# Performance work log

Measured on AMD Instinct MI355X. Metric: run time of the kernel, lower is better.

The kernel has to match this reference:

```python
import jax, jax.numpy as jnp
import numpy as np

B, T, D = 32, 1024, 1024
PCA_DIM = 256
NS = 4
NC = 1024
SEC = PCA_DIM // NS


def setup_inputs() -> dict:
    key = jax.random.key(0)
    k1, k2, k3 = jax.random.split(key, 3)
    inputs = jax.random.normal(k1, (B, T, D), dtype=jnp.float32)
    # variance_scaling(1.0, 'fan_avg', 'normal'): std = sqrt(2 / (fan_in + fan_out))
    pca_proj = jax.random.normal(k2, (D, PCA_DIM), dtype=jnp.float32) * np.float32(np.sqrt(2.0 / (D + PCA_DIM)))
    pre_bias = jnp.zeros((1, D), dtype=jnp.float32)
    # per-section codebooks, variance_scaling(0.1, 'fan_avg', 'normal')
    codebooks = jax.random.normal(k3, (NS, NC, SEC), dtype=jnp.float32) * np.float32(np.sqrt(0.1 * 2.0 / (NC + SEC)))
    return {"inputs": inputs, "pca_proj": pca_proj, "pre_bias": pre_bias, "codebooks": codebooks}


def reference(inputs, pca_proj, pre_bias, codebooks):
    in_shape = inputs.shape
    d = in_shape[-1]
    flat = inputs.reshape(-1, d)  # [N, D]
    n = flat.shape[0]
    # --- PCA projection + reconstruction / decorrelation losses ---
    projected = (flat + pre_bias) @ pca_proj            # [N, P]
    unprojected = projected @ pca_proj.T - pre_bias     # [N, D]
    l2_loss = jnp.mean(jnp.sqrt(jnp.sum(jnp.square(flat - unprojected), axis=-1)))
    cov = projected.T @ projected / n                   # [P, P]
    cov_loss = jnp.mean(jnp.square(cov - jnp.eye(pca_proj.shape[1], dtype=projected.dtype)))
    pca_loss = l2_loss + cov_loss
    # --- per-section vector quantization ---
    ns, nc, sec = codebooks.shape
    secs = projected.reshape(n, ns, sec).transpose(1, 0, 2)  # [ns, N, sec] == jnp.split along -1

    def quantize_section(x, cb):
        # x: [N, sec], cb: [nc, sec]; squared-L2 cdist via expansion
        dist = (jnp.sum(x * x, axis=1, keepdims=True)
                - 2.0 * (x @ cb.T)
                + jnp.sum(cb * cb, axis=1)[None, :])    # [N, nc]
        idx = jnp.argmin(dist, axis=1)                  # [N]
        q = cb[idx]                                     # gather == one_hot @ cb
        loss = jnp.square(q - jax.lax.stop_gradient(x))  # [N, sec]
        q_st = x + jax.lax.stop_gradient(q - x)         # straight-through
        return q_st, loss, idx

    q, sec_loss, idx = jax.vmap(quantize_section)(secs, codebooks)  # [ns,N,sec] x2, [ns,N]
    quantized = q.transpose(1, 0, 2).reshape(n, ns * sec)           # concat sections -> [N, P]
    quantized = (quantized @ pca_proj.T - pre_bias).reshape(in_shape)  # pca_unproject
    nn_idx = idx.reshape((ns,) + in_shape[:-1])                     # [ns, B, T]
    quantization_loss = jnp.mean(sec_loss.reshape((ns,) + in_shape[:-1] + (sec,)), axis=0) + pca_loss
    codebook = jax.lax.stop_gradient(codebooks.reshape(ns * nc, sec))
    cluster_counts = jnp.ones((ns, nc), dtype=jnp.float32)  # eval mode: jnp.ones init, no EMA
    return quantized, quantization_loss, nn_idx, codebook, cluster_counts
```

## Files before the change

### kernel.cpp

```cpp
#include <hip/hip_runtime.h>
#include <math.h>

#define NROW 32768
#define DIM  1024
#define PDIM 256
#define NSEC 4
#define NCODE 1024
#define SECD 64

__global__ __launch_bounds__(256) void k_proj(const float* __restrict__ X,
                                              const float* __restrict__ W,
                                              const float* __restrict__ bias,
                                              float* __restrict__ proj) {
    __shared__ float As[16][64];
    __shared__ float Bs[16][64];
    const int t = threadIdx.x;
    const int tx = t & 15, ty = t >> 4;
    const int rb = blockIdx.y * 64;
    const int cbase = blockIdx.x * 64;
    const int lr = t >> 2;
    const int lk = (t & 3) * 4;
    const int bk = t >> 4;
    const int bc = (t & 15) * 4;
    float acc[4][4] = {};
    float part[4][4] = {};
    for (int kc = 0; kc < DIM; kc += 16) {
        if (kc == 384) {
            #pragma unroll
            for (int i = 0; i < 4; ++i)
                #pragma unroll
                for (int j = 0; j < 4; ++j) { part[i][j] = acc[i][j]; acc[i][j] = 0.0f; }
        } else if (kc == 768) {
            #pragma unroll
            for (int i = 0; i < 4; ++i)
                #pragma unroll
                for (int j = 0; j < 4; ++j) { part[i][j] = __fadd_rn(part[i][j], acc[i][j]); acc[i][j] = 0.0f; }
        }
        float4 av = *(const float4*)&X[(size_t)(rb + lr) * DIM + kc + lk];
        float4 bb = *(const float4*)&bias[kc + lk];
        av.x += bb.x; av.y += bb.y; av.z += bb.z; av.w += bb.w;
        float4 bv = *(const float4*)&W[(size_t)(kc + bk) * PDIM + cbase + bc];
        As[lk + 0][lr] = av.x; As[lk + 1][lr] = av.y;
        As[lk + 2][lr] = av.z; As[lk + 3][lr] = av.w;
        *(float4*)&Bs[bk][bc] = bv;
        __syncthreads();
        #pragma unroll
        for (int k = 0; k < 16; ++k) {
            float4 a4 = *(const float4*)&As[k][ty * 4];
            float4 b4 = *(const float4*)&Bs[k][tx * 4];
            float aa[4] = {a4.x, a4.y, a4.z, a4.w};
            float bbv[4] = {b4.x, b4.y, b4.z, b4.w};
            #pragma unroll
            for (int i = 0; i < 4; ++i)
                #pragma unroll
                for (int j = 0; j < 4; ++j)
                    acc[i][j] = fmaf(aa[i], bbv[j], acc[i][j]);
        }
        __syncthreads();
    }
    #pragma unroll
    for (int i = 0; i < 4; ++i) {
        float r[4];
        #pragma unroll
        for (int j = 0; j < 4; ++j) r[j] = __fadd_rn(part[i][j], acc[i][j]);
        float4 v = make_float4(r[0], r[1], r[2], r[3]);
        *(float4*)&proj[(size_t)(rb + ty * 4 + i) * PDIM + cbase + tx * 4] = v;
    }
}

__global__ __launch_bounds__(256) void k_cov(const float* __restrict__ Pm,
                                             float* __restrict__ cov) {
    __shared__ float As[16][64];
    __shared__ float Bs[16][64];
    const int t = threadIdx.x;
    const int tx = t & 15, ty = t >> 4;
    const int ib = blockIdx.x * 64;
    const int jb = blockIdx.y * 64;
    const int nb = blockIdx.z * 2048;
    const int sk = t >> 4;
    const int sc = (t & 15) * 4;
    float acc[4][4] = {};
    for (int kc = 0; kc < 2048; kc += 16) {
        float4 a = *(const float4*)&Pm[(size_t)(nb + kc + sk) * PDIM + ib + sc];
        float4 b = *(const float4*)&Pm[(size_t)(nb + kc + sk) * PDIM + jb + sc];
        *(float4*)&As[sk][sc] = a;
        *(float4*)&Bs[sk][sc] = b;
        __syncthreads();
        #pragma unroll
        for (int k = 0; k < 16; ++k) {
            float4 a4 = *(const float4*)&As[k][ty * 4];
            float4 b4 = *(const float4*)&Bs[k][tx * 4];
            float aa[4] = {a4.x, a4.y, a4.z, a4.w};
            float bb[4] = {b4.x, b4.y, b4.z, b4.w};
            #pragma unroll
            for (int i = 0; i < 4; ++i)
                #pragma unroll
                for (int j = 0; j < 4; ++j)
                    acc[i][j] = fmaf(aa[i], bb[j], acc[i][j]);
        }
        __syncthreads();
    }
    #pragma unroll
    for (int i = 0; i < 4; ++i)
        #pragma unroll
        for (int j = 0; j < 4; ++j)
            atomicAdd(&cov[(size_t)(ib + ty * 4 + i) * PDIM + jb + tx * 4 + j], acc[i][j]);
}

__global__ __launch_bounds__(256) void k_covloss(const float* __restrict__ cov,
                                                 float* __restrict__ scal) {
    const int t = threadIdx.x;
    float s = 0.0f;
    for (int e = t; e < PDIM * PDIM; e += 256) {
        int i = e >> 8, j = e & 255;
        float v = cov[e] * (1.0f / 32768.0f) - (i == j ? 1.0f : 0.0f);
        s = fmaf(v, v, s);
    }
    #pragma unroll
    for (int o = 1; o < 64; o <<= 1) s += __shfl_xor(s, o);
    __shared__ float r4[4];
    if ((t & 63) == 0) r4[t >> 6] = s;
    __syncthreads();
    if (t == 0) scal[1] = (r4[0] + r4[1] + r4[2] + r4[3]) * (1.0f / 65536.0f);
}

__global__ __launch_bounds__(256) void k_unproj_res(const float* __restrict__ Pm,
                                                    const float* __restrict__ W,
                                                    const float* __restrict__ X,
                                                    const float* __restrict__ bias,
                                                    float* __restrict__ rowres) {
    __shared__ float As[16][64];
    __shared__ float Bs[16][64];
    const int t = threadIdx.x;
    const int tx = t & 15, ty = t >> 4;
    const int rb = blockIdx.y * 64;
    const int db = blockIdx.x * 64;
    const int lr = t >> 2;
    const int lk = (t & 3) * 4;
    float acc[4][4] = {};
    for (int kc = 0; kc < PDIM; kc += 16) {
        float4 a = *(const float4*)&Pm[(size_t)(rb + lr) * PDIM + kc + lk];
        float4 b = *(const float4*)&W[(size_t)(db + lr) * PDIM + kc + lk];
        As[lk + 0][lr] = a.x; As[lk + 1][lr] = a.y;
        As[lk + 2][lr] = a.z; As[lk + 3][lr] = a.w;
        Bs[lk + 0][lr] = b.x; Bs[lk + 1][lr] = b.y;
        Bs[lk + 2][lr] = b.z; Bs[lk + 3][lr] = b.w;
        __syncthreads();
        #pragma unroll
        for (int k = 0; k < 16; ++k) {
            float4 a4 = *(const float4*)&As[k][ty * 4];
            float4 b4 = *(const float4*)&Bs[k][tx * 4];
            float aa[4] = {a4.x, a4.y, a4.z, a4.w};
            float bb[4] = {b4.x, b4.y, b4.z, b4.w};
            #pragma unroll
            for (int i = 0; i < 4; ++i)
                #pragma unroll
                for (int j = 0; j < 4; ++j)
                    acc[i][j] = fmaf(aa[i], bb[j], acc[i][j]);
        }
        __syncthreads();
    }
    float4 b4 = *(const float4*)&bias[db + tx * 4];
    float bb[4] = {b4.x, b4.y, b4.z, b4.w};
    #pragma unroll
    for (int i = 0; i < 4; ++i) {
        const int row = rb + ty * 4 + i;
        float4 x4 = *(const float4*)&X[(size_t)row * DIM + db + tx * 4];
        float xx[4] = {x4.x, x4.y, x4.z, x4.w};
        float part = 0.0f;
        #pragma unroll
        for (int j = 0; j < 4; ++j) {
            float diff = xx[j] + bb[j] - acc[i][j];
            part = fmaf(diff, diff, part);
        }
        #pragma unroll
        for (int o = 1; o < 16; o <<= 1) part += __shfl_xor(part, o);
        if (tx == 0) atomicAdd(&rowres[row], part);
    }
}

__global__ __launch_bounds__(256) void k_l2(const float* __restrict__ rowres,
                                            float* __restrict__ scal) {
    int r = blockIdx.x * 256 + threadIdx.x;
    float v = sqrtf(rowres[r]);
    #pragma unroll
    for (int o = 1; o < 64; o <<= 1) v += __shfl_xor(v, o);
    if ((threadIdx.x & 63) == 0) atomicAdd(&scal[0], v);
}

__global__ __launch_bounds__(256) void k_cnorm(const float* __restrict__ cbs,
                                               float* __restrict__ cnorm) {
    int c = blockIdx.x * 256 + threadIdx.x;
    const float* p = &cbs[(size_t)c * SECD];
    float a[8];
    #pragma unroll
    for (int j = 0; j < 8; ++j) a[j] = __fmul_rn(p[j], p[j]);
    #pragma unroll
    for (int i = 8; i < 64; i += 8)
        #pragma unroll
        for (int j = 0; j < 8; ++j)
            a[j] = __fadd_rn(a[j], __fmul_rn(p[i + j], p[i + j]));
    float r = __fadd_rn(__fadd_rn(__fadd_rn(a[0], a[1]), __fadd_rn(a[2], a[3])),
                        __fadd_rn(__fadd_rn(a[4], a[5]), __fadd_rn(a[6], a[7])));
    cnorm[c] = r;
}

__global__ __launch_bounds__(256) void k_vq(const float* __restrict__ proj,
                                            const float* __restrict__ cbs,
                                            const float* __restrict__ cnorm,
                                            int* __restrict__ widx,
                                            float* __restrict__ out_idx,
                                            float* __restrict__ out_qloss) {
    __shared__ float xs[64][64];
    __shared__ float cs[64][64];
    __shared__ float xnorm[64];
    __shared__ int   sidx[64];
    __shared__ float qlds[64][65];
    const int t = threadIdx.x;
    const int tx = t & 15, ty = t >> 4;
    const int rb = blockIdx.x * 64;
    const int lr = t >> 2;
    const int kq = (t & 3) * 16;

    for (int e = t; e < 64 * 65; e += 256) (&qlds[0][0])[e] = 0.0f;

    for (int s = 0; s < NSEC; ++s) {
        #pragma unroll
        for (int i = 0; i < 16; i += 4) {
            float4 v = *(const float4*)&proj[(size_t)(rb + lr) * PDIM + s * SECD + kq + i];
            xs[kq + i + 0][lr] = v.x; xs[kq + i + 1][lr] = v.y;
            xs[kq + i + 2][lr] = v.z; xs[kq + i + 3][lr] = v.w;
        }
        __syncthreads();
        if (t < 64) {
            float a[8];
            #pragma unroll
            for (int j = 0; j < 8; ++j) { float v = xs[j][t]; a[j] = __fmul_rn(v, v); }
            #pragma unroll
            for (int i = 8; i < 64; i += 8)
                #pragma unroll
                for (int j = 0; j < 8; ++j) {
                    float v = xs[i + j][t];
                    a[j] = __fadd_rn(a[j], __fmul_rn(v, v));
                }
            xnorm[t] = __fadd_rn(__fadd_rn(__fadd_rn(a[0], a[1]), __fadd_rn(a[2], a[3])),
                                 __fadd_rn(__fadd_rn(a[4], a[5]), __fadd_rn(a[6], a[7])));
        }
        float best[4]; int bidx[4];
        #pragma unroll
        for (int i = 0; i < 4; ++i) { best[i] = 3.4e38f; bidx[i] = 0; }

        for (int ct = 0; ct < 16; ++ct) {
            __syncthreads();
            #pragma unroll
            for (int i = 0; i < 16; i += 4) {
                float4 v = *(const float4*)&cbs[(size_t)(s * NCODE + ct * 64 + lr) * SECD + kq + i];
                cs[kq + i + 0][lr] = v.x; cs[kq + i + 1][lr] = v.y;
                cs[kq + i + 2][lr] = v.z; cs[kq + i + 3][lr] = v.w;
            }
            __syncthreads();
            float4 cn4 = *(const float4*)&cnorm[s * NCODE + ct * 64 + tx * 4];
            float cna[4] = {cn4.x, cn4.y, cn4.z, cn4.w};
            float acc[4][4] = {};
            #pragma unroll 16
            for (int k = 0; k < 64; ++k) {
                float4 a4 = *(const float4*)&xs[k][ty * 4];
                float4 b4 = *(const float4*)&cs[k][tx * 4];
                float aa[4] = {a4.x, a4.y, a4.z, a4.w};
                float bb[4] = {b4.x, b4.y, b4.z, b4.w};
                #pragma unroll
                for (int i = 0; i < 4; ++i)
                    #pragma unroll
                    for (int j = 0; j < 4; ++j)
                        acc[i][j] = fmaf(aa[i], bb[j], acc[i][j]);
            }
            #pragma unroll
            for (int i = 0; i < 4; ++i) {
                float xn = xnorm[ty * 4 + i];
                #pragma unroll
                for (int j = 0; j < 4; ++j) {
                    float d = __fadd_rn(__fsub_rn(xn, __fmul_rn(2.0f, acc[i][j])), cna[j]);
                    int code = ct * 64 + tx * 4 + j;
                    if (d < best[i]) { best[i] = d; bidx[i] = code; }
                }
            }
        }
        #pragma unroll
        for (int i = 0; i < 4; ++i) {
            float d = best[i]; int ix = bidx[i];
            #pragma unroll
            for (int o = 1; o < 16; o <<= 1) {
                float od = __shfl_xor(d, o);
                int   oi = __shfl_xor(ix, o);
                if (od < d || (od == d && oi < ix)) { d = od; ix = oi; }
            }
            if (tx == 0) {
                int row = rb + ty * 4 + i;
                widx[s * NROW + row] = ix;
                out_idx[s * NROW + row] = (float)ix;
                sidx[ty * 4 + i] = ix;
            }
        }
        __syncthreads();
        {
            const float* crow = &cbs[(size_t)(s * NCODE + sidx[lr]) * SECD];
            #pragma unroll
            for (int i = 0; i < 16; i += 4) {
                float4 q = *(const float4*)&crow[kq + i];
                float qq[4] = {q.x, q.y, q.z, q.w};
                #pragma unroll
                for (int u = 0; u < 4; ++u) {
                    float d = qq[u] - xs[kq + i + u][lr];
                    qlds[lr][kq + i + u] += d * d;
                }
            }
        }
        __syncthreads();
    }
    for (int e = t; e < 4096; e += 256) {
        int r = e >> 6, j = e & 63;
        out_qloss[(size_t)(rb + r) * SECD + j] = 0.25f * qlds[r][j];
    }
}

__global__ __launch_bounds__(256) void k_cbu(const float* __restrict__ cbs,
                                             const float* __restrict__ W,
                                             float* __restrict__ cbu) {
    __shared__ float As[16][64];
    __shared__ float Bs[16][64];
    const int t = threadIdx.x;
    const int tx = t & 15, ty = t >> 4;
    const int s = blockIdx.z;
    const int cbase = blockIdx.y * 64;
    const int db = blockIdx.x * 64;
    const int lr = t >> 2;
    const int lk = (t & 3) * 4;
    float acc[4][4] = {};
    for (int kc = 0; kc < SECD; kc += 16) {
        float4 a = *(const float4*)&cbs[(size_t)(s * NCODE + cbase + lr) * SECD + kc + lk];
        float4 b = *(const float4*)&W[(size_t)(db + lr) * PDIM + s * SECD + kc + lk];
        As[lk + 0][lr] = a.x; As[lk + 1][lr] = a.y;
        As[lk + 2][lr] = a.z; As[lk + 3][lr] = a.w;
        Bs[lk + 0][lr] = b.x; Bs[lk + 1][lr] = b.y;
        Bs[lk + 2][lr] = b.z; Bs[lk + 3][lr] = b.w;
        __syncthreads();
        #pragma unroll
        for (int k = 0; k < 16; ++k) {
            float4 a4 = *(const float4*)&As[k][ty * 4];
            float4 b4 = *(const float4*)&Bs[k][tx * 4];
            float aa[4] = {a4.x, a4.y, a4.z, a4.w};
            float bb[4] = {b4.x, b4.y, b4.z, b4.w};
            #pragma unroll
            for (int i = 0; i < 4; ++i)
                #pragma unroll
                for (int j = 0; j < 4; ++j)
                    acc[i][j] = fmaf(aa[i], bb[j], acc[i][j]);
        }
        __syncthreads();
    }
    #pragma unroll
    for (int i = 0; i < 4; ++i) {
        float4 v = make_float4(acc[i][0], acc[i][1], acc[i][2], acc[i][3]);
        *(float4*)&cbu[(size_t)(s * NCODE + cbase + ty * 4 + i) * DIM + db + tx * 4] = v;
    }
}

__global__ __launch_bounds__(256) void k_gather(const float* __restrict__ cbu,
                                                const int* __restrict__ widx,
                                                const float* __restrict__ bias,
                                                float* __restrict__ out0) {
    const int n = blockIdx.x;
    const int d = threadIdx.x * 4;
    int i0 = widx[0 * NROW + n];
    int i1 = widx[1 * NROW + n];
    int i2 = widx[2 * NROW + n];
    int i3 = widx[3 * NROW + n];
    float4 v0 = *(const float4*)&cbu[((size_t)(0 * NCODE + i0)) * DIM + d];
    float4 v1 = *(const float4*)&cbu[((size_t)(1 * NCODE + i1)) * DIM + d];
    float4 v2 = *(const float4*)&cbu[((size_t)(2 * NCODE + i2)) * DIM + d];
    float4 v3 = *(const float4*)&cbu[((size_t)(3 * NCODE + i3)) * DIM + d];
    float4 b = *(const float4*)&bias[d];
    float4 r;
    r.x = v0.x + v1.x + v2.x + v3.x - b.x;
    r.y = v0.y + v1.y + v2.y + v3.y - b.y;
    r.z = v0.z + v1.z + v2.z + v3.z - b.z;
    r.w = v0.w + v1.w + v2.w + v3.w - b.w;
    *(float4*)&out0[(size_t)n * DIM + d] = r;
}

__global__ __launch_bounds__(256) void k_addpca(float* __restrict__ out1,
                                                const float* __restrict__ scal) {
    float pca = scal[0] * (1.0f / 32768.0f) + scal[1];
    int e = blockIdx.x * 256 + threadIdx.x;
    float4* p = (float4*)out1;
    float4 v = p[e];
    v.x += pca; v.y += pca; v.z += pca; v.w += pca;
    p[e] = v;
}

__global__ __launch_bounds__(256) void k_tail(const float* __restrict__ cbs,
                                              float* __restrict__ out3,
                                              float* __restrict__ out4) {
    int e = blockIdx.x * 256 + threadIdx.x;
    ((float4*)out3)[e] = ((const float4*)cbs)[e];
    if (e < 4096) out4[e] = 1.0f;
}

extern "C" void kernel_launch(void* const* d_in, const int* in_sizes, int n_in,
                              void* d_out, int out_size, void* d_ws, size_t ws_size,
                              hipStream_t stream) {
    (void)in_sizes; (void)n_in; (void)out_size; (void)ws_size;
    const float* X    = (const float*)d_in[0];
    const float* W    = (const float*)d_in[1];
    const float* bias = (const float*)d_in[2];
    const float* cbs  = (const float*)d_in[3];

    float* out  = (float*)d_out;
    float* out0 = out;
    float* out1 = out + 33554432;
    float* out2 = out + 35651584;
    float* out3 = out + 35782656;
    float* out4 = out + 36044800;

    char* ws = (char*)d_ws;
    float* cbu    = (float*)(ws);
    float* rowres = (float*)(ws + 16777216);
    float* cov    = (float*)(ws + 16908288);
    float* scal   = (float*)(ws + 17170432);
    float* cnorm  = (float*)(ws + 17170496);
    int*   widx   = (int*)  (ws + 17186880);

    float* proj = out0;

    hipMemsetAsync(ws + 16777216, 0, 131072 + 262144 + 64, stream);

    k_proj      <<<dim3(4, 512),    256, 0, stream>>>(X, W, bias, proj);
    k_cov       <<<dim3(4, 4, 16),  256, 0, stream>>>(proj, cov);
    k_covloss   <<<1,               256, 0, stream>>>(cov, scal);
    k_unproj_res<<<dim3(16, 512),   256, 0, stream>>>(proj, W, X, bias, rowres);
    k_l2        <<<128,             256, 0, stream>>>(rowres, scal);
    k_cnorm     <<<16,              256, 0, stream>>>(cbs, cnorm);
    k_vq        <<<512,             256, 0, stream>>>(proj, cbs, cnorm, widx, out2, out1);
    k_cbu       <<<dim3(16, 16, 4), 256, 0, stream>>>(cbs, W, cbu);
    k_gather    <<<32768,           256, 0, stream>>>(cbu, widx, bias, out0);
    k_addpca    <<<2048,            256, 0, stream>>>(out1, scal);
    k_tail      <<<256,             256, 0, stream>>>(cbs, out3, out4);
}
```

Measured before the change: 1.278 ms.

## Compute reconstruction residual via W^T W Gram expansion and enlarge GEMM tiles

Replaces the full N×D unprojection GEMM for the l2 loss with the expansion ||x||² − 2p·p + p·(p WᵀW), computed as a small WᵀW Gram matrix, a 256×256 GEMM per row block, and row-wise reductions. This removes a 1024-wide reconstruction GEMM and its re-read of X. The projection GEMM moves to 128×128 tiles with 8×8 per-thread register blocking, and the VQ kernel to 128-code tiles with the loss accumulated in registers instead of shared memory. The expanded form can lose precision through cancellation, which may change the l2 loss slightly, and the larger tiles raise register pressure.

New measurement: 1.265 ms. About the same (-1.0%).

```diff
diff --git a/kernel.cpp b/kernel.cpp
--- a/kernel.cpp
+++ b/kernel.cpp
@@ -12,60 +12,193 @@
                                               const float* __restrict__ W,
                                               const float* __restrict__ bias,
                                               float* __restrict__ proj) {
+    __shared__ float As[16][128];
+    __shared__ float Bs[16][128];
+    const int t = threadIdx.x;
+    const int ry = t >> 4;
+    const int rx = t & 15;
+    const int rb = blockIdx.y * 128;
+    const int cb = blockIdx.x * 128;
+    const int lr = t >> 1;
+    const int lk = (t & 1) * 8;
+    const int bk = t >> 4;
+    const int bc = (t & 15) * 8;
+    float acc[8][8] = {};
+    float part[8][8] = {};
+    for (int kc = 0; kc < DIM; kc += 16) {
+        if (kc == 384) {
+            #pragma unroll
+            for (int i = 0; i < 8; ++i)
+                #pragma unroll
+                for (int j = 0; j < 8; ++j) { part[i][j] = acc[i][j]; acc[i][j] = 0.0f; }
+        } else if (kc == 768) {
+            #pragma unroll
+            for (int i = 0; i < 8; ++i)
+                #pragma unroll
+                for (int j = 0; j < 8; ++j) { part[i][j] = __fadd_rn(part[i][j], acc[i][j]); acc[i][j] = 0.0f; }
+        }
+        float4 a0 = *(const float4*)&X[(size_t)(rb + lr) * DIM + kc + lk];
+        float4 a1 = *(const float4*)&X[(size_t)(rb + lr) * DIM + kc + lk + 4];
+        float4 c0 = *(const float4*)&bias[kc + lk];
+        float4 c1 = *(const float4*)&bias[kc + lk + 4];
+        a0.x += c0.x; a0.y += c0.y; a0.z += c0.z; a0.w += c0.w;
+        a1.x += c1.x; a1.y += c1.y; a1.z += c1.z; a1.w += c1.w;
+        float4 b0 = *(const float4*)&W[(size_t)(kc + bk) * PDIM + cb + bc];
+        float4 b1 = *(const float4*)&W[(size_t)(kc + bk) * PDIM + cb + bc + 4];
+        As[lk + 0][lr] = a0.x; As[lk + 1][lr] = a0.y; As[lk + 2][lr] = a0.z; As[lk + 3][lr] = a0.w;
+        As[lk + 4][lr] = a1.x; As[lk + 5][lr] = a1.y; As[lk + 6][lr] = a1.z; As[lk + 7][lr] = a1.w;
+        *(float4*)&Bs[bk][bc] = b0;
+        *(float4*)&Bs[bk][bc + 4] = b1;
+        __syncthreads();
+        #pragma unroll
+        for (int k = 0; k < 16; ++k) {
+            float4 x0 = *(const float4*)&As[k][ry * 8];
+            float4 x1 = *(const float4*)&As[k][ry * 8 + 4];
+            float4 y0 = *(const float4*)&Bs[k][rx * 8];
+            float4 y1 = *(const float4*)&Bs[k][rx * 8 + 4];
+            float aa[8] = {x0.x, x0.y, x0.z, x0.w, x1.x, x1.y, x1.z, x1.w};
+            float bb[8] = {y0.x, y0.y, y0.z, y0.w, y1.x, y1.y, y1.z, y1.w};
+            #pragma unroll
+            for (int i = 0; i < 8; ++i)
+                #pragma unroll
+                for (int j = 0; j < 8; ++j)
+                    acc[i][j] = fmaf(aa[i], bb[j], acc[i][j]);
+        }
+        __syncthreads();
+    }
+    #pragma unroll
+    for (int i = 0; i < 8; ++i) {
+        float r[8];
+        #pragma unroll
+        for (int j = 0; j < 8; ++j) r[j] = __fadd_rn(part[i][j], acc[i][j]);
+        const size_t base = (size_t)(rb + ry * 8 + i) * PDIM + cb + rx * 8;
+        *(float4*)&proj[base]     = make_float4(r[0], r[1], r[2], r[3]);
+        *(float4*)&proj[base + 4] = make_float4(r[4], r[5], r[6], r[7]);
+    }
+}
+
+__global__ __launch_bounds__(256) void k_pm(const float* __restrict__ P,
+                                            const float* __restrict__ M,
+                                            float* __restrict__ PM) {
+    __shared__ float As[16][128];
+    __shared__ float Bs[16][128];
+    const int t = threadIdx.x;
+    const int ry = t >> 4;
+    const int rx = t & 15;
+    const int rb = blockIdx.y * 128;
+    const int cb = blockIdx.x * 128;
+    const int lr = t >> 1;
+    const int lk = (t & 1) * 8;
+    const int bk = t >> 4;
+    const int bc = (t & 15) * 8;
+    float acc[8][8] = {};
+    for (int kc = 0; kc < PDIM; kc += 16) {
+        float4 a0 = *(const float4*)&P[(size_t)(rb + lr) * PDIM + kc + lk];
+        float4 a1 = *(const float4*)&P[(size_t)(rb + lr) * PDIM + kc + lk + 4];
+        float4 b0 = *(const float4*)&M[(size_t)(kc + bk) * PDIM + cb + bc];
+        float4 b1 = *(const float4*)&M[(size_t)(kc + bk) * PDIM + cb + bc + 4];
+        As[lk + 0][lr] = a0.x; As[lk + 1][lr] = a0.y; As[lk + 2][lr] = a0.z; As[lk + 3][lr] = a0.w;
+        As[lk + 4][lr] = a1.x; As[lk + 5][lr] = a1.y; As[lk + 6][lr] = a1.z; As[lk + 7][lr] = a1.w;
+        *(float4*)&Bs[bk][bc] = b0;
+        *(float4*)&Bs[bk][bc + 4] = b1;
+        __syncthreads();
+        #pragma unroll
+        for (int k = 0; k < 16; ++k) {
+            float4 x0 = *(const float4*)&As[k][ry * 8];
+            float4 x1 = *(const float4*)&As[k][ry * 8 + 4];
+            float4 y0 = *(const float4*)&Bs[k][rx * 8];
+            float4 y1 = *(const float4*)&Bs[k][rx * 8 + 4];
+            float aa[8] = {x0.x, x0.y, x0.z, x0.w, x1.x, x1.y, x1.z, x1.w};
+            float bb[8] = {y0.x, y0.y, y0.z, y0.w, y1.x, y1.y, y1.z, y1.w};
+            #pragma unroll
+            for (int i = 0; i < 8; ++i)
+                #pragma unroll
+                for (int j = 0; j < 8; ++j)
+                    acc[i][j] = fmaf(aa[i], bb[j], acc[i][j]);
+        }
+        __syncthreads();
+    }
+    #pragma unroll
+    for (int i = 0; i < 8; ++i) {
+        const size_t base = (size_t)(rb + ry * 8 + i) * PDIM + cb + rx * 8;
+        *(float4*)&PM[base]     = make_float4(acc[i][0], acc[i][1], acc[i][2], acc[i][3]);
+        *(float4*)&PM[base + 4] = make_float4(acc[i][4], acc[i][5], acc[i][6], acc[i][7]);
+    }
+}
+
+__global__ __launch_bounds__(256) void k_wtw(const float* __restrict__ W,
+                                             float* __restrict__ M) {
     __shared__ float As[16][64];
     __shared__ float Bs[16][64];
     const int t = threadIdx.x;
     const int tx = t & 15, ty = t >> 4;
-    const int rb = blockIdx.y * 64;
-    const int cbase = blockIdx.x * 64;
-    const int lr = t >> 2;
-    const int lk = (t & 3) * 4;
-    const int bk = t >> 4;
-    const int bc = (t & 15) * 4;
+    const int ib = blockIdx.x * 64;
+    const int jb = blockIdx.y * 64;
+    const int sk = t >> 4;
+    const int sc = (t & 15) * 4;
     float acc[4][4] = {};
-    float part[4][4] = {};
     for (int kc = 0; kc < DIM; kc += 16) {
-        if (kc == 384) {
-            #pragma unroll
-            for (int i = 0; i < 4; ++i)
-                #pragma unroll
-                for (int j = 0; j < 4; ++j) { part[i][j] = acc[i][j]; acc[i][j] = 0.0f; }
-        } else if (kc == 768) {
-            #pragma unroll
-            for (int i = 0; i < 4; ++i)
-                #pragma unroll
-                for (int j = 0; j < 4; ++j) { part[i][j] = __fadd_rn(part[i][j], acc[i][j]); acc[i][j] = 0.0f; }
-        }
-        float4 av = *(const float4*)&X[(size_t)(rb + lr) * DIM + kc + lk];
-        float4 bb = *(const float4*)&bias[kc + lk];
-        av.x += bb.x; av.y += bb.y; av.z += bb.z; av.w += bb.w;
-        float4 bv = *(const float4*)&W[(size_t)(kc + bk) * PDIM + cbase + bc];
-        As[lk + 0][lr] = av.x; As[lk + 1][lr] = av.y;
-        As[lk + 2][lr] = av.z; As[lk + 3][lr] = av.w;
-        *(float4*)&Bs[bk][bc] = bv;
+        float4 a = *(const float4*)&W[(size_t)(kc + sk) * PDIM + ib + sc];
+        float4 b = *(const float4*)&W[(size_t)(kc + sk) * PDIM + jb + sc];
+        *(float4*)&As[sk][sc] = a;
+        *(float4*)&Bs[sk][sc] = b;
         __syncthreads();
         #pragma unroll
         for (int k = 0; k < 16; ++k) {
             float4 a4 = *(const float4*)&As[k][ty * 4];
             float4 b4 = *(const float4*)&Bs[k][tx * 4];
             float aa[4] = {a4.x, a4.y, a4.z, a4.w};
-            float bbv[4] = {b4.x, b4.y, b4.z, b4.w};
+            float bb[4] = {b4.x, b4.y, b4.z, b4.w};
             #pragma unroll
             for (int i = 0; i < 4; ++i)
                 #pragma unroll
                 for (int j = 0; j < 4; ++j)
-                    acc[i][j] = fmaf(aa[i], bbv[j], acc[i][j]);
-        }
-        __syncthreads();
-    }
+                    acc[i][j] = fmaf(aa[i], bb[j], acc[i][j]);
+        }
+        __syncthreads();
+    }
+    #pragma unroll
+    for (int i = 0; i < 4; ++i)
+        #pragma unroll
+        for (int j = 0; j < 4; ++j)
+            M[(size_t)(ib + ty * 4 + i) * PDIM + jb + tx * 4 + j] = acc[i][j];
+}
+
+__global__ __launch_bounds__(256) void k_xn2(const float* __restrict__ X,
+                                             const float* __restrict__ bias,
+                                             float* __restrict__ xn2) {
+    const int n = blockIdx.x * 4 + (threadIdx.x >> 6);
+    const int lane = threadIdx.x & 63;
+    float s = 0.0f;
     #pragma unroll
     for (int i = 0; i < 4; ++i) {
-        float r[4];
-        #pragma unroll
-        for (int j = 0; j < 4; ++j) r[j] = __fadd_rn(part[i][j], acc[i][j]);
-        float4 v = make_float4(r[0], r[1], r[2], r[3]);
-        *(float4*)&proj[(size_t)(rb + ty * 4 + i) * PDIM + cbase + tx * 4] = v;
-    }
+        float4 x = *(const float4*)&X[(size_t)n * DIM + i * 256 + lane * 4];
+        float4 b = *(const float4*)&bias[i * 256 + lane * 4];
+        float vx = x.x + b.x, vy = x.y + b.y, vz = x.z + b.z, vw = x.w + b.w;
+        s = fmaf(vx, vx, s); s = fmaf(vy, vy, s);
+        s = fmaf(vz, vz, s); s = fmaf(vw, vw, s);
+    }
+    #pragma unroll
+    for (int o = 1; o < 64; o <<= 1) s += __shfl_xor(s, o);
+    if (lane == 0) xn2[n] = s;
+}
+
+__global__ __launch_bounds__(256) void k_rowres(const float* __restrict__ P,
+                                                const float* __restrict__ PM,
+                                                const float* __restrict__ xn2,
+                                                float* __restrict__ rowres) {
+    const int n = blockIdx.x * 4 + (threadIdx.x >> 6);
+    const int lane = threadIdx.x & 63;
+    float4 p  = *(const float4*)&P[(size_t)n * PDIM + lane * 4];
+    float4 pm = *(const float4*)&PM[(size_t)n * PDIM + lane * 4];
+    float s = 0.0f;
+    s = fmaf(p.x, pm.x - 2.0f * p.x, s);
+    s = fmaf(p.y, pm.y - 2.0f * p.y, s);
+    s = fmaf(p.z, pm.z - 2.0f * p.z, s);
+    s = fmaf(p.w, pm.w - 2.0f * p.w, s);
+    #pragma unroll
+    for (int o = 1; o < 64; o <<= 1) s += __shfl_xor(s, o);
+    if (lane == 0) rowres[n] = xn2[n] + s;
 }
 
 __global__ __launch_bounds__(256) void k_cov(const float* __restrict__ Pm,
@@ -124,61 +257,6 @@
     if (t == 0) scal[1] = (r4[0] + r4[1] + r4[2] + r4[3]) * (1.0f / 65536.0f);
 }
 
-__global__ __launch_bounds__(256) void k_unproj_res(const float* __restrict__ Pm,
-                                                    const float* __restrict__ W,
-                                                    const float* __restrict__ X,
-                                                    const float* __restrict__ bias,
-                                                    float* __restrict__ rowres) {
-    __shared__ float As[16][64];
-    __shared__ float Bs[16][64];
-    const int t = threadIdx.x;
-    const int tx = t & 15, ty = t >> 4;
-    const int rb = blockIdx.y * 64;
-    const int db = blockIdx.x * 64;
-    const int lr = t >> 2;
-    const int lk = (t & 3) * 4;
-    float acc[4][4] = {};
-    for (int kc = 0; kc < PDIM; kc += 16) {
-        float4 a = *(const float4*)&Pm[(size_t)(rb + lr) * PDIM + kc + lk];
-        float4 b = *(const float4*)&W[(size_t)(db + lr) * PDIM + kc + lk];
-        As[lk + 0][lr] = a.x; As[lk + 1][lr] = a.y;
-        As[lk + 2][lr] = a.z; As[lk + 3][lr] = a.w;
-        Bs[lk + 0][lr] = b.x; Bs[lk + 1][lr] = b.y;
-        Bs[lk + 2][lr] = b.z; Bs[lk + 3][lr] = b.w;
-        __syncthreads();
-        #pragma unroll
-        for (int k = 0; k < 16; ++k) {
-            float4 a4 = *(const float4*)&As[k][ty * 4];
-            float4 b4 = *(const float4*)&Bs[k][tx * 4];
-            float aa[4] = {a4.x, a4.y, a4.z, a4.w};
-            float bb[4] = {b4.x, b4.y, b4.z, b4.w};
-            #pragma unroll
-            for (int i = 0; i < 4; ++i)
-                #pragma unroll
-                for (int j = 0; j < 4; ++j)
-                    acc[i][j] = fmaf(aa[i], bb[j], acc[i][j]);
-        }
-        __syncthreads();
-    }
-    float4 b4 = *(const float4*)&bias[db + tx * 4];
-    float bb[4] = {b4.x, b4.y, b4.z, b4.w};
-    #pragma unroll
-    for (int i = 0; i < 4; ++i) {
-        const int row = rb + ty * 4 + i;
-        float4 x4 = *(const float4*)&X[(size_t)row * DIM + db + tx * 4];
-        float xx[4] = {x4.x, x4.y, x4.z, x4.w};
-        float part = 0.0f;
-        #pragma unroll
-        for (int j = 0; j < 4; ++j) {
-            float diff = xx[j] + bb[j] - acc[i][j];
-            part = fmaf(diff, diff, part);
-        }
-        #pragma unroll
-        for (int o = 1; o < 16; o <<= 1) part += __shfl_xor(part, o);
-        if (tx == 0) atomicAdd(&rowres[row], part);
-    }
-}
-
 __global__ __launch_bounds__(256) void k_l2(const float* __restrict__ rowres,
                                             float* __restrict__ scal) {
     int r = blockIdx.x * 256 + threadIdx.x;
@@ -212,17 +290,20 @@
                                             float* __restrict__ out_idx,
                                             float* __restrict__ out_qloss) {
     __shared__ float xs[64][64];
-    __shared__ float cs[64][64];
+    __shared__ float cs[64][128];
     __shared__ float xnorm[64];
     __shared__ int   sidx[64];
-    __shared__ float qlds[64][65];
-    const int t = threadIdx.x;
-    const int tx = t & 15, ty = t >> 4;
+    const int t = threadIdx.x;
+    const int ry = t >> 5;
+    const int tx = t & 31;
     const int rb = blockIdx.x * 64;
     const int lr = t >> 2;
     const int kq = (t & 3) * 16;
-
-    for (int e = t; e < 64 * 65; e += 256) (&qlds[0][0])[e] = 0.0f;
+    const int cr = t >> 1;
+    const int ko = (t & 1) * 32;
+    float qacc[16];
+    #pragma unroll
+    for (int i = 0; i < 16; ++i) qacc[i] = 0.0f;
 
     for (int s = 0; s < NSEC; ++s) {
         #pragma unroll
@@ -246,59 +327,60 @@
             xnorm[t] = __fadd_rn(__fadd_rn(__fadd_rn(a[0], a[1]), __fadd_rn(a[2], a[3])),
                                  __fadd_rn(__fadd_rn(a[4], a[5]), __fadd_rn(a[6], a[7])));
         }
-        float best[4]; int bidx[4];
-        #pragma unroll
-        for (int i = 0; i < 4; ++i) { best[i] = 3.4e38f; bidx[i] = 0; }
-
-        for (int ct = 0; ct < 16; ++ct) {
+        float best[8]; int bidx[8];
+        #pragma unroll
+        for (int i = 0; i < 8; ++i) { best[i] = 3.4e38f; bidx[i] = 0; }
+
+        for (int ct = 0; ct < 8; ++ct) {
             __syncthreads();
             #pragma unroll
-            for (int i = 0; i < 16; i += 4) {
-                float4 v = *(const float4*)&cbs[(size_t)(s * NCODE + ct * 64 + lr) * SECD + kq + i];
-                cs[kq + i + 0][lr] = v.x; cs[kq + i + 1][lr] = v.y;
-                cs[kq + i + 2][lr] = v.z; cs[kq + i + 3][lr] = v.w;
+            for (int u = 0; u < 32; u += 4) {
+                float4 v = *(const float4*)&cbs[(size_t)(s * NCODE + ct * 128 + cr) * SECD + ko + u];
+                cs[ko + u + 0][cr] = v.x; cs[ko + u + 1][cr] = v.y;
+                cs[ko + u + 2][cr] = v.z; cs[ko + u + 3][cr] = v.w;
             }
             __syncthreads();
-            float4 cn4 = *(const float4*)&cnorm[s * NCODE + ct * 64 + tx * 4];
+            float4 cn4 = *(const float4*)&cnorm[s * NCODE + ct * 128 + tx * 4];
             float cna[4] = {cn4.x, cn4.y, cn4.z, cn4.w};
-            float acc[4][4] = {};
-            #pragma unroll 16
+            float acc[8][4] = {};
+            #pragma unroll 8
             for (int k = 0; k < 64; ++k) {
-                float4 a4 = *(const float4*)&xs[k][ty * 4];
+                float4 x0 = *(const float4*)&xs[k][ry * 8];
+                float4 x1 = *(const float4*)&xs[k][ry * 8 + 4];
                 float4 b4 = *(const float4*)&cs[k][tx * 4];
-                float aa[4] = {a4.x, a4.y, a4.z, a4.w};
+                float aa[8] = {x0.x, x0.y, x0.z, x0.w, x1.x, x1.y, x1.z, x1.w};
                 float bb[4] = {b4.x, b4.y, b4.z, b4.w};
                 #pragma unroll
-                for (int i = 0; i < 4; ++i)
+                for (int i = 0; i < 8; ++i)
                     #pragma unroll
                     for (int j = 0; j < 4; ++j)
                         acc[i][j] = fmaf(aa[i], bb[j], acc[i][j]);
             }
             #pragma unroll
-            for (int i = 0; i < 4; ++i) {
-                float xn = xnorm[ty * 4 + i];
+            for (int i = 0; i < 8; ++i) {
+                float xn = xnorm[ry * 8 + i];
                 #pragma unroll
                 for (int j = 0; j < 4; ++j) {
                     float d = __fadd_rn(__fsub_rn(xn, __fmul_rn(2.0f, acc[i][j])), cna[j]);
-                    int code = ct * 64 + tx * 4 + j;
+                    int code = ct * 128 + tx * 4 + j;
                     if (d < best[i]) { best[i] = d; bidx[i] = code; }
                 }
             }
         }
         #pragma unroll
-        for (int i = 0; i < 4; ++i) {
+        for (int i = 0; i < 8; ++i) {
             float d = best[i]; int ix = bidx[i];
             #pragma unroll
-            for (int o = 1; o < 16; o <<= 1) {
+            for (int o = 1; o < 32; o <<= 1) {
                 float od = __shfl_xor(d, o);
                 int   oi = __shfl_xor(ix, o);
                 if (od < d || (od == d && oi < ix)) { d = od; ix = oi; }
             }
             if (tx == 0) {
-                int row = rb + ty * 4 + i;
+                int row = rb + ry * 8 + i;
                 widx[s * NROW + row] = ix;
                 out_idx[s * NROW + row] = (float)ix;
-                sidx[ty * 4 + i] = ix;
+                sidx[ry * 8 + i] = ix;
             }
         }
         __syncthreads();
@@ -311,15 +393,17 @@
                 #pragma unroll
                 for (int u = 0; u < 4; ++u) {
                     float d = qq[u] - xs[kq + i + u][lr];
-                    qlds[lr][kq + i + u] += d * d;
+                    qacc[i + u] = fmaf(d, d, qacc[i + u]);
                 }
             }
         }
         __syncthreads();
     }
-    for (int e = t; e < 4096; e += 256) {
-        int r = e >> 6, j = e & 63;
-        out_qloss[(size_t)(rb + r) * SECD + j] = 0.25f * qlds[r][j];
+    #pragma unroll
+    for (int i = 0; i < 16; i += 4) {
+        float4 v = make_float4(0.25f * qacc[i + 0], 0.25f * qacc[i + 1],
+                               0.25f * qacc[i + 2], 0.25f * qacc[i + 3]);
+        *(float4*)&out_qloss[(size_t)(rb + lr) * SECD + kq + i] = v;
     }
 }
 
@@ -429,20 +513,26 @@
     float* scal   = (float*)(ws + 17170432);
     float* cnorm  = (float*)(ws + 17170496);
     int*   widx   = (int*)  (ws + 17186880);
+    float* wtw    = (float*)(ws + 17711168);
 
     float* proj = out0;
-
-    hipMemsetAsync(ws + 16777216, 0, 131072 + 262144 + 64, stream);
-
-    k_proj      <<<dim3(4, 512),    256, 0, stream>>>(X, W, bias, proj);
-    k_cov       <<<dim3(4, 4, 16),  256, 0, stream>>>(proj, cov);
-    k_covloss   <<<1,               256, 0, stream>>>(cov, scal);
-    k_unproj_res<<<dim3(16, 512),   256, 0, stream>>>(proj, W, X, bias, rowres);
-    k_l2        <<<128,             256, 0, stream>>>(rowres, scal);
-    k_cnorm     <<<16,              256, 0, stream>>>(cbs, cnorm);
-    k_vq        <<<512,             256, 0, stream>>>(proj, cbs, cnorm, widx, out2, out1);
-    k_cbu       <<<dim3(16, 16, 4), 256, 0, stream>>>(cbs, W, cbu);
-    k_gather    <<<32768,           256, 0, stream>>>(cbu, widx, bias, out0);
-    k_addpca    <<<2048,            256, 0, stream>>>(out1, scal);
-    k_tail      <<<256,             256, 0, stream>>>(cbs, out3, out4);
-}
+    float* PM   = out0 + 16777216;
+    float* xn2  = out0 + 25165824;
+
+    hipMemsetAsync(ws + 16908288, 0, 262144 + 64, stream);
+
+    k_proj    <<<dim3(2, 256),    256, 0, stream>>>(X, W, bias, proj);
+    k_xn2     <<<8192,            256, 0, stream>>>(X, bias, xn2);
+    k_wtw     <<<dim3(4, 4),      256, 0, stream>>>(W, wtw);
+    k_cov     <<<dim3(4, 4, 16),  256, 0, stream>>>(proj, cov);
+    k_covloss <<<1,               256, 0, stream>>>(cov, scal);
+    k_pm      <<<dim3(2, 256),    256, 0, stream>>>(proj, wtw, PM);
+    k_rowres  <<<8192,            256, 0, stream>>>(proj, PM, xn2, rowres);
+    k_l2      <<<128,             256, 0, stream>>>(rowres, scal);
+    k_cnorm   <<<16,              256, 0, stream>>>(cbs, cnorm);
+    k_vq      <<<512,             256, 0, stream>>>(proj, cbs, cnorm, widx, out2, out1);
+    k_cbu     <<<dim3(16, 16, 4), 256, 0, stream>>>(cbs, W, cbu);
+    k_gather  <<<32768,           256, 0, stream>>>(cbu, widx, bias, out0);
+    k_addpca  <<<2048,            256, 0, stream>>>(out1, scal);
+    k_tail    <<<256,             256, 0, stream>>>(cbs, out3, out4);
+}
```
